# Kernel optimization log

Measured on AMD Instinct MI355X. Metric: run time of the kernel, lower is better.

## Reference

```python
import jax, jax.numpy as jnp
import numpy as np

EPS = 1e-5
K = 20


def _bn(x, gamma, beta):
    # BatchNorm in training mode: stats over all axes except last (channel)
    axes = tuple(range(x.ndim - 1))
    m = jnp.mean(x, axes, keepdims=True)
    v = jnp.var(x, axes, keepdims=True)
    return gamma * (x - m) * jax.lax.rsqrt(v + EPS) + beta


def _leaky(x):
    return jax.nn.leaky_relu(x, 0.2)


def _edge_conv(x, W, gamma, beta):
    # x: [B, N, C] channel-last. Faithful to source: topk on cdist with
    # torch default largest=True (k FARTHEST points). Squared distance
    # preserves the ordering of euclidean distance.
    sq = jnp.sum(x * x, axis=-1)                                    # [B,N]
    d2 = sq[:, :, None] + sq[:, None, :] - 2.0 * jnp.einsum('bnc,bmc->bnm', x, x)
    idx = jax.lax.top_k(d2, K)[1]                                   # [B,N,K]
    nbr = jax.vmap(lambda xi, ii: xi[ii])(x, idx)                   # [B,N,K,C]
    ctr = jnp.broadcast_to(x[:, :, None, :], nbr.shape)
    feat = jnp.concatenate([nbr - ctr, ctr], axis=-1)               # [B,N,K,2C]
    h = jnp.einsum('bnkc,oc->bnko', feat, W)                        # 1x1 conv
    return jnp.max(_leaky(_bn(h, gamma, beta)), axis=2)             # [B,N,O]


def _plane(x, w1, g1, b1, w2, g2, b2, w3, g3, b3, w4, g4, b4,
           w5, g5, b5, wl1, g6, b6, wl2, bl2, g7, b7):
    xt = jnp.transpose(x, (0, 2, 1))                                # [B,N,3]
    h1 = _edge_conv(xt, w1, g1, b1)                                 # [B,N,64]
    h2 = _edge_conv(h1, w2, g2, b2)                                 # [B,N,64]
    h3 = _edge_conv(h2, w3, g3, b3)                                 # [B,N,128]
    h4 = _edge_conv(h3, w4, g4, b4)                                 # [B,N,256]
    hc = jnp.concatenate([h1, h2, h3, h4], axis=-1)                 # [B,N,512]
    h = _leaky(_bn(jnp.einsum('bnc,oc->bno', hc, w5), g5, b5))      # [B,N,1024]
    pooled = jnp.concatenate([jnp.max(h, axis=1), jnp.mean(h, axis=1)], axis=-1)  # [B,2048]
    h = _leaky(_bn(pooled @ wl1.T, g6, b6))                         # [B,512]
    h = _leaky(_bn(h @ wl2.T + bl2, g7, b7))                        # [B,256]
    return h  # dropout p=0.0 -> identity


def setup_inputs() -> dict:
    key = jax.random.key(0)
    ks = jax.random.split(key, 16)
    B, N = 8, 2048
    f32 = jnp.float32
    d = {
        'x0': jax.random.normal(ks[0], (B, 3, N), f32),
        'x1': jax.random.normal(ks[1], (B, 3, N), f32),
        'x2': jax.random.normal(ks[2], (B, 3, N), f32),
        'w1': jax.random.normal(ks[3], (64, 6), f32) * 0.3,
        'w2': jax.random.normal(ks[4], (64, 128), f32) * 0.08,
        'w3': jax.random.normal(ks[5], (128, 128), f32) * 0.08,
        'w4': jax.random.normal(ks[6], (256, 256), f32) * 0.06,
        'w5': jax.random.normal(ks[7], (1024, 512), f32) * 0.04,
        'wl1': jax.random.normal(ks[8], (512, 2048), f32) * 0.02,
        'wl2': jax.random.normal(ks[9], (256, 512), f32) * 0.04,
        'bl2': jnp.zeros((256,), f32),
        'whead': jax.random.normal(ks[10], (7, 768), f32) * 0.03,
        'bhead': jnp.zeros((7,), f32),
    }
    for name, c in [('1', 64), ('2', 64), ('3', 128), ('4', 256), ('5', 1024),
                    ('6', 512), ('7', 256), ('8', 7)]:
        d['g' + name] = jnp.ones((c,), f32)
        d['b' + name] = jnp.zeros((c,), f32)
    return d


def reference(x0, x1, x2, w1, g1, b1, w2, g2, b2, w3, g3, b3, w4, g4, b4,
              w5, g5, b5, wl1, g6, b6, wl2, bl2, g7, b7, whead, bhead, g8, b8):
    feats = [
        _plane(x, w1, g1, b1, w2, g2, b2, w3, g3, b3, w4, g4, b4,
               w5, g5, b5, wl1, g6, b6, wl2, bl2, g7, b7)
        for x in (x0, x1, x2)
    ]
    h = jnp.concatenate(feats, axis=-1)                             # [B,768]
    # final MLP head: 1x1 conv on [B,768,1] + BN1d + ReLU + squeeze
    out = jnp.einsum('bc,oc->bo', h, whead) + bhead                 # [B,7]
    out = jax.nn.relu(_bn(out, g8, b8))
    return out
```

## Files before the change

kernel.cpp:

```cpp
#include <hip/hip_runtime.h>
#include <hip/hip_bf16.h>
#include <cstdint>
#include <cstddef>

constexpr int NB = 8;
constexpr int NP = 2048;
constexpr int BN = NB * NP;
constexpr int KK = 20;
constexpr float EPSBN = 1e-5f;
constexpr float NEG = -3.402823466e38f;
constexpr int SLOTS = 8;
constexpr int SLOTSM = 32;
constexpr int SLOTSW = 8;

typedef __attribute__((ext_vector_type(8))) short bf16x8;
typedef __attribute__((ext_vector_type(16))) float f32x16;

__device__ __forceinline__ float leaky(float x) { return x > 0.f ? x : 0.2f * x; }

__device__ __forceinline__ void split2(float x, unsigned short& h, unsigned short& l) {
    __hip_bfloat16 hh = __float2bfloat16(x);
    float hf = __bfloat162float(hh);
    __hip_bfloat16 ll = __float2bfloat16(x - hf);
    h = *reinterpret_cast<unsigned short*>(&hh);
    l = *reinterpret_cast<unsigned short*>(&ll);
}

__device__ __forceinline__ float b2f(unsigned short u) {
    __hip_bfloat16 h = *reinterpret_cast<__hip_bfloat16*>(&u);
    return __bfloat162float(h);
}

__device__ __forceinline__ unsigned int f2key(float f) {
    unsigned int u = __float_as_uint(f);
    return u ^ (unsigned int)(((int)u >> 31) | 0x80000000);
}

__global__ void k_transpose(const float* __restrict__ x, float* __restrict__ xt) {
    int i = blockIdx.x * 256 + threadIdx.x;
    if (i >= BN) return;
    int b = i >> 11, n = i & 2047;
    float4 v;
    v.x = x[(b * 3 + 0) * NP + n];
    v.y = x[(b * 3 + 1) * NP + n];
    v.z = x[(b * 3 + 2) * NP + n];
    v.w = 0.f;
    *(float4*)&xt[(size_t)i * 4] = v;
}

template <int CP4>
__global__ void k_sq4(const float4* __restrict__ FT4, float* __restrict__ sq) {
    int i = blockIdx.x * 256 + threadIdx.x;
    if (i >= BN) return;
    float s = 0.f;
#pragma unroll
    for (int cq = 0; cq < CP4; ++cq) {
        float4 f = FT4[(size_t)cq * BN + i];
        s += f.x * f.x + f.y * f.y + f.z * f.z + f.w * f.w;
    }
    sq[i] = s;
}

template <int CP>
__launch_bounds__(512, 4)
__global__ void k_knn2(const float4* __restrict__ FT4, const float* __restrict__ sq,
                       int* __restrict__ gidx) {
    constexpr int R = 8;
    constexpr int CP4 = CP / 4;
    __shared__ unsigned int ds[R][NP];
    int t = threadIdx.x;
    int b = blockIdx.x >> 8;
    int n0 = (blockIdx.x & 255) * R;
    const float4* FTb = FT4 + (size_t)b * NP;
    const float* sqb = sq + (size_t)b * NP;

    float acc[R][4];
#pragma unroll
    for (int r = 0; r < R; ++r)
#pragma unroll
        for (int mi = 0; mi < 4; ++mi) acc[r][mi] = 0.f;

    for (int cq = 0; cq < CP4; ++cq) {
        float4 f[4];
#pragma unroll
        for (int mi = 0; mi < 4; ++mi)
            f[mi] = FTb[(size_t)cq * BN + t + mi * 512];
#pragma unroll
        for (int r = 0; r < R; ++r) {
            float4 cv = FTb[(size_t)cq * BN + n0 + r];
#pragma unroll
            for (int mi = 0; mi < 4; ++mi)
                acc[r][mi] += f[mi].x * cv.x + f[mi].y * cv.y + f[mi].z * cv.z + f[mi].w * cv.w;
        }
    }
#pragma unroll
    for (int mi = 0; mi < 4; ++mi) {
        int m = t + mi * 512;
        float sm = sqb[m];
#pragma unroll
        for (int r = 0; r < R; ++r) ds[r][m] = f2key(sm - 2.f * acc[r][mi]);
    }
    __syncthreads();

    int wave = t >> 6, lane = t & 63;
    unsigned long long below = (1ull << lane) - 1ull;
    {
        int r = wave;
        unsigned int kv[32];
#pragma unroll
        for (int j = 0; j < 32; ++j) kv[j] = ds[r][lane + 64 * j];

        unsigned int T = 0;
        bool exact = false;
#pragma unroll 1
        for (int bit = 31; bit >= 0; --bit) {
            unsigned int tt = T | (1u << bit);
            int c = 0;
#pragma unroll
            for (int j = 0; j < 32; ++j)
                c += (int)__popcll(__ballot(kv[j] >= tt));
            if (c >= KK) {
                T = tt;
                if (c == KK) { exact = true; break; }
            }
        }

        int obase = (b * NP + n0 + r) * KK;
        if (exact) {
            int base = 0;
#pragma unroll 1
            for (int j = 0; j < 32; ++j) {
                bool pg = kv[j] >= T;
                unsigned long long mk = __ballot(pg);
                if (pg) gidx[obase + base + (int)__popcll(mk & below)] = lane + 64 * j;
                base += (int)__popcll(mk);
            }
        } else {
            int base = 0;
#pragma unroll 1
            for (int j = 0; j < 32; ++j) {
                bool pg = kv[j] > T;
                unsigned long long mk = __ballot(pg);
                if (pg) gidx[obase + base + (int)__popcll(mk & below)] = lane + 64 * j;
                base += (int)__popcll(mk);
            }
            int rem = KK - base;
#pragma unroll 1
            for (int j = 0; j < 32; ++j) {
                if (rem <= 0) break;
                bool pe = kv[j] == T;
                unsigned long long mk = __ballot(pe);
                int myp = (int)__popcll(mk & below);
                if (pe && myp < rem) gidx[obase + base + myp] = lane + 64 * j;
                int cnt = (int)__popcll(mk);
                int take = cnt < rem ? cnt : rem;
                base += take; rem -= take;
            }
        }
    }
}

__global__ void k_prepw(const float* __restrict__ W, int O, int Cact, int CP,
                        float* __restrict__ WaT, float* __restrict__ WdT) {
    int i = blockIdx.x * 256 + threadIdx.x;
    if (i >= CP * O) return;
    int c = i / O, o = i % O;
    float wa = (c < Cact) ? W[o * 2 * Cact + c] : 0.f;
    float wb = (c < Cact) ? W[o * 2 * Cact + Cact + c] : 0.f;
    WaT[i] = wa;
    WdT[i] = wb - wa;
}

__global__ void k_prepws2(const float* __restrict__ W, int O, int C,
                          unsigned short* __restrict__ WcH, unsigned short* __restrict__ WcL) {
    int i = blockIdx.x * 256 + threadIdx.x;
    if (i >= 2 * O * C) return;
    int r = i / C, k = i % C;
    float v;
    if (r < O) v = W[r * 2 * C + k];
    else {
        int o = r - O;
        v = W[o * 2 * C + C + k] - W[o * 2 * C + k];
    }
    split2(v, WcH[i], WcL[i]);
}

__global__ void k_splitw5(const float* __restrict__ w5, unsigned short* __restrict__ w5H,
                          unsigned short* __restrict__ w5L) {
    int i = blockIdx.x * 256 + threadIdx.x;
    if (i >= 1024 * 512) return;
    split2(w5[i], w5H[i], w5L[i]);
}

template <int O, int CP>
__launch_bounds__(O)
__global__ void k_conv(const float* __restrict__ F, int ld, const int* __restrict__ gidx,
                       const float* __restrict__ WaT, const float* __restrict__ WdT,
                       float* __restrict__ hmax, float* __restrict__ s1p,
                       float* __restrict__ s2p) {
    constexpr int CP4 = CP / 4;
    __shared__ float nbrT[2][CP][32];
    __shared__ float sctr[2][CP];
    __shared__ int sidx[2][KK];
    int t = threadIdx.x;
    int p0 = blockIdx.x * 2;
    int b = p0 >> 11;
    const float* Fb = F + (size_t)b * NP * ld;

    if (t < 2 * KK) {
        int pt = t / KK, k = t % KK;
        sidx[pt][k] = gidx[(size_t)(p0 + pt) * KK + k];
    }
    for (int e = t; e < 2 * CP; e += O) {
        int pt = e / CP, cc = e % CP;
        int n = (p0 + pt) & 2047;
        sctr[pt][cc] = Fb[(size_t)n * ld + cc];
    }
    __syncthreads();
    for (int e = t; e < 2 * KK * CP4; e += O) {
        int pt = e / (KK * CP4);
        int e2 = e % (KK * CP4);
        int k = e2 / CP4, cq = e2 % CP4;
        float4 f = *(const float4*)&Fb[(size_t)sidx[pt][k] * ld + cq * 4];
        int kp = (k + 4 * (cq & 7)) & 31;
        nbrT[pt][cq * 4 + 0][kp] = f.x;
        nbrT[pt][cq * 4 + 1][kp] = f.y;
        nbrT[pt][cq * 4 + 2][kp] = f.z;
        nbrT[pt][cq * 4 + 3][kp] = f.w;
    }
    __syncthreads();

    int o = t;
    float bacc0 = 0.f, bacc1 = 0.f;
#pragma unroll 4
    for (int c = 0; c < CP; ++c) {
        float w = WdT[c * O + o];
        bacc0 += sctr[0][c] * w;
        bacc1 += sctr[1][c] * w;
    }
    float a0[KK], a1[KK];
#pragma unroll
    for (int k = 0; k < KK; ++k) { a0[k] = 0.f; a1[k] = 0.f; }
#pragma unroll 2
    for (int c = 0; c < CP; ++c) {
        float w = WaT[c * O + o];
        int s = 4 * ((c >> 2) & 7);
#pragma unroll
        for (int kq = 0; kq < KK / 4; ++kq) {
            int kp = (4 * kq + s) & 31;
            float4 f0 = *(const float4*)&nbrT[0][c][kp];
            float4 f1 = *(const float4*)&nbrT[1][c][kp];
            a0[kq * 4 + 0] += w * f0.x; a1[kq * 4 + 0] += w * f1.x;
            a0[kq * 4 + 1] += w * f0.y; a1[kq * 4 + 1] += w * f1.y;
            a0[kq * 4 + 2] += w * f0.z; a1[kq * 4 + 2] += w * f1.z;
            a0[kq * 4 + 3] += w * f0.w; a1[kq * 4 + 3] += w * f1.w;
        }
    }
    float hm0 = NEG, hm1 = NEG, ts1 = 0.f, ts2 = 0.f;
#pragma unroll
    for (int k = 0; k < KK; ++k) {
        float h0 = a0[k] + bacc0;
        float h1 = a1[k] + bacc1;
        hm0 = fmaxf(hm0, h0); hm1 = fmaxf(hm1, h1);
        ts1 += h0 + h1; ts2 += h0 * h0 + h1 * h1;
    }
    hmax[(size_t)p0 * O + o] = hm0;
    hmax[(size_t)(p0 + 1) * O + o] = hm1;
    int slot = blockIdx.x & (SLOTS - 1);
    atomicAdd(&s1p[slot * O + o], ts1);
    atomicAdd(&s2p[slot * O + o], ts2);
}

template <int O, int C, int COFF>
__launch_bounds__(256, 4)
__global__ void k_gemms(const unsigned short* __restrict__ hcH,
                        const unsigned short* __restrict__ hcL,
                        const unsigned short* __restrict__ WdH,
                        const unsigned short* __restrict__ WdL,
                        float* __restrict__ bacc) {
    constexpr int KS = C / 16;
    int tid = threadIdx.x, wave = tid >> 6, lane = tid & 63;
    int row = lane & 31, half = lane >> 5;
    int p0 = blockIdx.x * 128 + wave * 32;
    int ob = blockIdx.y * 64;
    const unsigned short* aH = hcH + (size_t)(p0 + row) * 512 + COFF;
    const unsigned short* aL = hcL + (size_t)(p0 + row) * 512 + COFF;
    f32x16 acc[2];
#pragma unroll
    for (int nt = 0; nt < 2; ++nt)
#pragma unroll
        for (int r = 0; r < 16; ++r) acc[nt][r] = 0.f;

#pragma unroll 2
    for (int ks = 0; ks < KS; ++ks) {
        int k0 = ks * 16 + half * 8;
        bf16x8 avh = *(const bf16x8*)(aH + k0);
        bf16x8 avl = *(const bf16x8*)(aL + k0);
#pragma unroll
        for (int nt = 0; nt < 2; ++nt) {
            int j = ob + nt * 32 + row;
            bf16x8 bvh = *(const bf16x8*)(WdH + (size_t)j * C + k0);
            bf16x8 bvl = *(const bf16x8*)(WdL + (size_t)j * C + k0);
            acc[nt] = __builtin_amdgcn_mfma_f32_32x32x16_bf16(avh, bvh, acc[nt], 0, 0, 0);
            acc[nt] = __builtin_amdgcn_mfma_f32_32x32x16_bf16(avh, bvl, acc[nt], 0, 0, 0);
            acc[nt] = __builtin_amdgcn_mfma_f32_32x32x16_bf16(avl, bvh, acc[nt], 0, 0, 0);
        }
    }
#pragma unroll
    for (int nt = 0; nt < 2; ++nt)
#pragma unroll
        for (int r = 0; r < 16; ++r) {
            int i = (r & 3) + 8 * (r >> 2) + 4 * half;
            bacc[(size_t)(p0 + i) * O + ob + nt * 32 + row] = acc[nt][r];
        }
}

template <int O>
__launch_bounds__(256)
__global__ void k_gmax(const float* __restrict__ Gz, const int* __restrict__ gidx,
                       float* __restrict__ hmax, float* __restrict__ s1p,
                       float* __restrict__ s2p) {
    constexpr int PB = 256 / O;
    constexpr int O2 = 2 * O;
    __shared__ int sidx[PB][KK];
    int t = threadIdx.x;
    int pt = t / O, o = t % O;
    int p0 = blockIdx.x * PB;
    if (t < PB * KK) sidx[t / KK][t % KK] = gidx[(size_t)(p0 + t / KK) * KK + t % KK];
    __syncthreads();

    int p = p0 + pt;
    int b = p >> 11;
    const float* Gb = Gz + (size_t)b * 2048 * O2;
    float bacc = Gz[(size_t)p * O2 + O + o];
    float mx = NEG, ts1 = 0.f, ts2 = 0.f;
#pragma unroll 5
    for (int k = 0; k < KK; ++k) {
        float g = Gb[(size_t)sidx[pt][k] * O2 + o];
        float h = g + bacc;
        mx = fmaxf(mx, g);
        ts1 += h; ts2 += h * h;
    }
    hmax[(size_t)p * O + o] = mx + bacc;
    int slot = blockIdx.x & (SLOTSM - 1);
    atomicAdd(&s1p[slot * O + o], ts1);
    atomicAdd(&s2p[slot * O + o], ts2);
}

__global__ void k_redslots(const float* __restrict__ s1p, const float* __restrict__ s2p,
                           int O, int S, float* __restrict__ s1g, float* __restrict__ s2g) {
    int o = blockIdx.x * 256 + threadIdx.x;
    if (o >= O) return;
    float a = 0.f, c = 0.f;
    for (int s = 0; s < S; ++s) { a += s1p[s * O + o]; c += s2p[s * O + o]; }
    s1g[o] = a; s2g[o] = c;
}

__global__ void k_bnmax(const float* __restrict__ hmax, int O, const float* __restrict__ s1g,
                        const float* __restrict__ s2g, const float* __restrict__ gam,
                        const float* __restrict__ bet, unsigned short* __restrict__ outH,
                        unsigned short* __restrict__ outL, int ostride, int ooff,
                        float inv_cnt) {
    int i = blockIdx.x * 256 + threadIdx.x;
    if (i >= BN * O) return;
    int o = i % O, p = i / O;
    float m = s1g[o] * inv_cnt;
    float v = s2g[o] * inv_cnt - m * m;
    float rs = rsqrtf(v + EPSBN);
    float y = leaky(gam[o] * (hmax[i] - m) * rs + bet[o]);
    size_t oi = (size_t)p * ostride + ooff + o;
    split2(y, outH[oi], outL[oi]);
}

__global__ void k_pack4(const unsigned short* __restrict__ inH,
                        const unsigned short* __restrict__ inL, int coff,
                        float4* __restrict__ out) {
    __shared__ float tile[64][65];
    int tx = threadIdx.x & 63, ty = threadIdx.x >> 6;
    int p0 = blockIdx.x * 64, o0 = blockIdx.y * 64;
    for (int i = ty; i < 64; i += 4) {
        size_t idx = (size_t)(p0 + i) * 512 + coff + o0 + tx;
        tile[i][tx] = b2f(inH[idx]) + b2f(inL[idx]);
    }
    __syncthreads();
    for (int q = ty; q < 16; q += 4) {
        float4 v;
        v.x = tile[tx][4 * q + 0];
        v.y = tile[tx][4 * q + 1];
        v.z = tile[tx][4 * q + 2];
        v.w = tile[tx][4 * q + 3];
        out[(size_t)(o0 / 4 + q) * BN + p0 + tx] = v;
    }
}

__launch_bounds__(256, 2)
__global__ void k_w5ms(const unsigned short* __restrict__ hcH,
                       const unsigned short* __restrict__ hcL,
                       const unsigned short* __restrict__ w5H,
                       const unsigned short* __restrict__ w5L,
                       float* __restrict__ g5, float* __restrict__ s1p,
                       float* __restrict__ s2p) {
    int tid = threadIdx.x, wave = tid >> 6, lane = tid & 63;
    int row = lane & 31, half = lane >> 5;
    int p0 = blockIdx.x * 64;
    int ob = blockIdx.y * 512 + wave * 128;
    const unsigned short* aH0 = hcH + (size_t)(p0 + row) * 512;
    const unsigned short* aL0 = hcL + (size_t)(p0 + row) * 512;
    const unsigned short* aH1 = hcH + (size_t)(p0 + 32 + row) * 512;
    const unsigned short* aL1 = hcL + (size_t)(p0 + 32 + row) * 512;
    f32x16 acc0[4], acc1[4];
#pragma unroll
    for (int nt = 0; nt < 4; ++nt)
#pragma unroll
        for (int r = 0; r < 16; ++r) { acc0[nt][r] = 0.f; acc1[nt][r] = 0.f; }

#pragma unroll 2
    for (int ks = 0; ks < 32; ++ks) {
        int k0 = ks * 16 + half * 8;
        bf16x8 avh0 = *(const bf16x8*)(aH0 + k0);
        bf16x8 avl0 = *(const bf16x8*)(aL0 + k0);
        bf16x8 avh1 = *(const bf16x8*)(aH1 + k0);
        bf16x8 avl1 = *(const bf16x8*)(aL1 + k0);
#pragma unroll
        for (int nt = 0; nt < 4; ++nt) {
            int j = ob + nt * 32 + row;
            bf16x8 bvh = *(const bf16x8*)(w5H + (size_t)j * 512 + k0);
            bf16x8 bvl = *(const bf16x8*)(w5L + (size_t)j * 512 + k0);
            acc0[nt] = __builtin_amdgcn_mfma_f32_32x32x16_bf16(avh0, bvh, acc0[nt], 0, 0, 0);
            acc0[nt] = __builtin_amdgcn_mfma_f32_32x32x16_bf16(avh0, bvl, acc0[nt], 0, 0, 0);
            acc0[nt] = __builtin_amdgcn_mfma_f32_32x32x16_bf16(avl0, bvh, acc0[nt], 0, 0, 0);
            acc1[nt] = __builtin_amdgcn_mfma_f32_32x32x16_bf16(avh1, bvh, acc1[nt], 0, 0, 0);
            acc1[nt] = __builtin_amdgcn_mfma_f32_32x32x16_bf16(avh1, bvl, acc1[nt], 0, 0, 0);
            acc1[nt] = __builtin_amdgcn_mfma_f32_32x32x16_bf16(avl1, bvh, acc1[nt], 0, 0, 0);
        }
    }
    int slot = blockIdx.x & (SLOTSW - 1);
#pragma unroll
    for (int nt = 0; nt < 4; ++nt) {
        int j = ob + nt * 32 + row;
        float s10 = 0.f, s20 = 0.f, s11 = 0.f, s21 = 0.f;
#pragma unroll
        for (int r = 0; r < 16; ++r) {
            int i = (r & 3) + 8 * (r >> 2) + 4 * half;
            float v0 = acc0[nt][r];
            float v1 = acc1[nt][r];
            g5[(size_t)(p0 + i) * 1024 + j] = v0;
            g5[(size_t)(p0 + 32 + i) * 1024 + j] = v1;
            s10 += v0; s20 += v0 * v0;
            s11 += v1; s21 += v1 * v1;
        }
        s10 += __shfl_xor(s10, 32);
        s20 += __shfl_xor(s20, 32);
        s11 += __shfl_xor(s11, 32);
        s21 += __shfl_xor(s21, 32);
        if (half == 0) {
            atomicAdd(&s1p[slot * 1024 + j], s10 + s11);
            atomicAdd(&s2p[slot * 1024 + j], s20 + s21);
        }
    }
}

__global__ void k_pool(const float* __restrict__ gbuf, const float* __restrict__ s1g,
                       const float* __restrict__ s2g, const float* __restrict__ gam,
                       const float* __restrict__ bet, float* __restrict__ pmax,
                       float* __restrict__ psum) {
    int t = threadIdx.x;
    int blk = blockIdx.x;
    int nc = blk & 7, ot = (blk >> 3) & 3, b = blk >> 5;
    int o = ot * 256 + t;
    float m = s1g[o] * (1.f / 16384.f);
    float v = s2g[o] * (1.f / 16384.f) - m * m;
    float rs = rsqrtf(v + EPSBN);
    float ga = gam[o], be = bet[o];
    float vmax = NEG, vsum = 0.f;
    for (int j = 0; j < 256; ++j) {
        int n = nc * 256 + j;
        float x = gbuf[((size_t)b * NP + n) * 1024 + o];
        float y = leaky(ga * (x - m) * rs + be);
        vmax = fmaxf(vmax, y);
        vsum += y;
    }
    pmax[(b * 1024 + o) * 8 + nc] = vmax;
    psum[(b * 1024 + o) * 8 + nc] = vsum;
}

__global__ void k_poolfin(const float* __restrict__ pmax, const float* __restrict__ psum,
                          float* __restrict__ pooled) {
    int i = blockIdx.x * 256 + threadIdx.x;
    if (i >= 8192) return;
    float mx = NEG, sm = 0.f;
    for (int j = 0; j < 8; ++j) {
        mx = fmaxf(mx, pmax[i * 8 + j]);
        sm += psum[i * 8 + j];
    }
    int b = i >> 10, o = i & 1023;
    pooled[b * 2048 + o] = mx;
    pooled[b * 2048 + 1024 + o] = sm * (1.f / 2048.f);
}

template <int CIN>
__global__ void k_fc(const float* __restrict__ in, const float* __restrict__ W,
                     const float* __restrict__ bias, int O, float* __restrict__ z) {
    int i = blockIdx.x * 256 + threadIdx.x;
    if (i >= NB * O) return;
    int b = i / O, o = i % O;
    const float* wr = W + (size_t)o * CIN;
    const float* ir = in + (size_t)b * CIN;
    float acc = 0.f;
#pragma unroll 4
    for (int cq = 0; cq < CIN / 4; ++cq) {
        float4 wv = *(const float4*)&wr[cq * 4];
        float4 iv = *(const float4*)&ir[cq * 4];
        acc += wv.x * iv.x + wv.y * iv.y + wv.z * iv.z + wv.w * iv.w;
    }
    z[i] = acc + (bias ? bias[o] : 0.f);
}

__global__ void k_bnb(const float* __restrict__ z, int O, const float* __restrict__ gam,
                      const float* __restrict__ bet, float* __restrict__ out, int ostride,
                      int ooff) {
    int o = blockIdx.x * 256 + threadIdx.x;
    if (o >= O) return;
    float s1 = 0.f, s2 = 0.f;
#pragma unroll
    for (int b = 0; b < NB; ++b) {
        float x = z[b * O + o];
        s1 += x; s2 += x * x;
    }
    float m = s1 * 0.125f, v = s2 * 0.125f - m * m;
    float rs = rsqrtf(v + EPSBN);
    float ga = gam[o], be = bet[o];
    for (int b = 0; b < NB; ++b) {
        float y = ga * (z[b * O + o] - m) * rs + be;
        out[b * ostride + ooff + o] = leaky(y);
    }
}

__global__ void k_head(const float* __restrict__ hf, const float* __restrict__ wh,
                       const float* __restrict__ bh, const float* __restrict__ g8,
                       const float* __restrict__ b8, float* __restrict__ out) {
    __shared__ float zh[56];
    int t = threadIdx.x;
    if (t < 56) {
        int b = t / 7, o = t % 7;
        float acc = bh[o];
        for (int c = 0; c < 768; ++c) acc += hf[b * 768 + c] * wh[o * 768 + c];
        zh[t] = acc;
    }
    __syncthreads();
    if (t < 7) {
        float s1 = 0.f, s2 = 0.f;
        for (int b = 0; b < NB; ++b) {
            float x = zh[b * 7 + t];
            s1 += x; s2 += x * x;
        }
        float m = s1 * 0.125f, v = s2 * 0.125f - m * m;
        float rs = rsqrtf(v + EPSBN);
        for (int b = 0; b < NB; ++b) {
            float y = g8[t] * (zh[b * 7 + t] - m) * rs + b8[t];
            out[b * 7 + t] = fmaxf(y, 0.f);
        }
    }
}

extern "C" void kernel_launch(void* const* d_in, const int* in_sizes, int n_in, void* d_out,
                              int out_size, void* d_ws, size_t ws_size, hipStream_t stream) {
    const float* x[3] = {(const float*)d_in[0], (const float*)d_in[1], (const float*)d_in[2]};
    const float* w1 = (const float*)d_in[3];
    const float* w2 = (const float*)d_in[4];
    const float* w3 = (const float*)d_in[5];
    const float* w4 = (const float*)d_in[6];
    const float* w5 = (const float*)d_in[7];
    const float* wl1 = (const float*)d_in[8];
    const float* wl2 = (const float*)d_in[9];
    const float* bl2 = (const float*)d_in[10];
    const float* whead = (const float*)d_in[11];
    const float* bhead = (const float*)d_in[12];
    const float *g1 = (const float*)d_in[13], *b1 = (const float*)d_in[14];
    const float *g2 = (const float*)d_in[15], *b2 = (const float*)d_in[16];
    const float *g3 = (const float*)d_in[17], *b3 = (const float*)d_in[18];
    const float *g4 = (const float*)d_in[19], *b4 = (const float*)d_in[20];
    const float *g5 = (const float*)d_in[21], *b5 = (const float*)d_in[22];
    const float *g6 = (const float*)d_in[23], *b6 = (const float*)d_in[24];
    const float *g7 = (const float*)d_in[25], *b7 = (const float*)d_in[26];
    const float *g8 = (const float*)d_in[27], *b8 = (const float*)d_in[28];

    char* w = (char*)d_ws;
    auto alloc = [&](size_t bytes) {
        char* p = w;
        w += (bytes + 255) & ~(size_t)255;
        return p;
    };
    float* xt   = (float*)alloc((size_t)BN * 4 * 4);
    unsigned short* hcH = (unsigned short*)alloc((size_t)BN * 512 * 2);
    unsigned short* hcL = (unsigned short*)alloc((size_t)BN * 512 * 2);
    float4* ft4 = (float4*)alloc((size_t)32 * BN * 16);
    float* gbig = (float*)alloc((size_t)BN * 1024 * 4);
    int*   idx  = (int*)alloc((size_t)BN * KK * 4);
    float* sqv  = (float*)alloc((size_t)BN * 4);
    float* s1g  = (float*)alloc(1024 * 4);
    float* s2g  = (float*)alloc(1024 * 4);
    float* spart  = (float*)alloc(2 * SLOTS * 256 * 4);
    float* spartC = (float*)alloc(2 * SLOTSM * 256 * 4);
    float* spartW = (float*)alloc(2 * SLOTSW * 1024 * 4);
    float* pmax = (float*)alloc(8 * 1024 * 8 * 4);
    float* psum = (float*)alloc(8 * 1024 * 8 * 4);
    float* pooled = (float*)alloc(8 * 2048 * 4);
    float* z1 = (float*)alloc(8 * 512 * 4);
    float* a1 = (float*)alloc(8 * 512 * 4);
    float* z2 = (float*)alloc(8 * 256 * 4);
    float* hfeat = (float*)alloc(8 * 768 * 4);
    float* Wa1 = (float*)alloc(4 * 64 * 4);
    float* Wd1 = (float*)alloc(4 * 64 * 4);
    unsigned short* WcH2 = (unsigned short*)alloc(128 * 64 * 2);
    unsigned short* WcL2 = (unsigned short*)alloc(128 * 64 * 2);
    unsigned short* WcH3 = (unsigned short*)alloc(256 * 64 * 2);
    unsigned short* WcL3 = (unsigned short*)alloc(256 * 64 * 2);
    unsigned short* WcH4 = (unsigned short*)alloc(512 * 128 * 2);
    unsigned short* WcL4 = (unsigned short*)alloc(512 * 128 * 2);
    unsigned short* w5H  = (unsigned short*)alloc(1024 * 512 * 2);
    unsigned short* w5L  = (unsigned short*)alloc(1024 * 512 * 2);
    float* s1p = spart;
    float* s2p = spart + SLOTS * 256;
    float* s1pc = spartC;
    float* s2pc = spartC + SLOTSM * 256;
    float* s1pw = spartW;
    float* s2pw = spartW + SLOTSW * 1024;
    float* hmaxP = gbig + (size_t)BN * 512;

    k_prepw<<<(4 * 64 + 255) / 256, 256, 0, stream>>>(w1, 64, 3, 4, Wa1, Wd1);
    k_prepws2<<<(128 * 64 + 255) / 256, 256, 0, stream>>>(w2, 64, 64, WcH2, WcL2);
    k_prepws2<<<(256 * 64 + 255) / 256, 256, 0, stream>>>(w3, 128, 64, WcH3, WcL3);
    k_prepws2<<<(512 * 128 + 255) / 256, 256, 0, stream>>>(w4, 256, 128, WcH4, WcL4);
    k_splitw5<<<(1024 * 512) / 256, 256, 0, stream>>>(w5, w5H, w5L);

    const float inv_e = 1.f / (float)(BN * KK);
    for (int p = 0; p < 3; ++p) {
        k_transpose<<<BN / 256, 256, 0, stream>>>(x[p], xt);

        k_sq4<1><<<BN / 256, 256, 0, stream>>>((const float4*)xt, sqv);
        k_knn2<4><<<NB * (NP / 8), 512, 0, stream>>>((const float4*)xt, sqv, idx);
        hipMemsetAsync(spart, 0, 2 * SLOTS * 256 * 4, stream);
        k_conv<64, 4><<<BN / 2, 64, 0, stream>>>(xt, 4, idx, Wa1, Wd1, hmaxP, s1p, s2p);
        k_redslots<<<1, 256, 0, stream>>>(s1p, s2p, 64, SLOTS, s1g, s2g);
        k_bnmax<<<(BN * 64) / 256, 256, 0, stream>>>(hmaxP, 64, s1g, s2g, g1, b1, hcH, hcL, 512, 0, inv_e);
        k_pack4<<<dim3(BN / 64, 1), 256, 0, stream>>>(hcH, hcL, 0, ft4);

        k_sq4<16><<<BN / 256, 256, 0, stream>>>(ft4, sqv);
        k_knn2<64><<<NB * (NP / 8), 512, 0, stream>>>(ft4, sqv, idx);
        k_gemms<128, 64, 0><<<dim3(BN / 128, 2), 256, 0, stream>>>(hcH, hcL, WcH2, WcL2, gbig);
        hipMemsetAsync(spartC, 0, 2 * SLOTSM * 256 * 4, stream);
        k_gmax<64><<<BN / 4, 256, 0, stream>>>(gbig, idx, hmaxP, s1pc, s2pc);
        k_redslots<<<1, 256, 0, stream>>>(s1pc, s2pc, 64, SLOTSM, s1g, s2g);
        k_bnmax<<<(BN * 64) / 256, 256, 0, stream>>>(hmaxP, 64, s1g, s2g, g2, b2, hcH, hcL, 512, 64, inv_e);
        k_pack4<<<dim3(BN / 64, 1), 256, 0, stream>>>(hcH, hcL, 64, ft4);

        k_sq4<16><<<BN / 256, 256, 0, stream>>>(ft4, sqv);
        k_knn2<64><<<NB * (NP / 8), 512, 0, stream>>>(ft4, sqv, idx);
        k_gemms<256, 64, 64><<<dim3(BN / 128, 4), 256, 0, stream>>>(hcH, hcL, WcH3, WcL3, gbig);
        hipMemsetAsync(spartC, 0, 2 * SLOTSM * 256 * 4, stream);
        k_gmax<128><<<BN / 2, 256, 0, stream>>>(gbig, idx, hmaxP, s1pc, s2pc);
        k_redslots<<<1, 256, 0, stream>>>(s1pc, s2pc, 128, SLOTSM, s1g, s2g);
        k_bnmax<<<(BN * 128) / 256, 256, 0, stream>>>(hmaxP, 128, s1g, s2g, g3, b3, hcH, hcL, 512, 128, inv_e);
        k_pack4<<<dim3(BN / 64, 2), 256, 0, stream>>>(hcH, hcL, 128, ft4);

        k_sq4<32><<<BN / 256, 256, 0, stream>>>(ft4, sqv);
        k_knn2<128><<<NB * (NP / 8), 512, 0, stream>>>(ft4, sqv, idx);
        k_gemms<512, 128, 128><<<dim3(BN / 128, 8), 256, 0, stream>>>(hcH, hcL, WcH4, WcL4, gbig);
        hipMemsetAsync(spartC, 0, 2 * SLOTSM * 256 * 4, stream);
        k_gmax<256><<<BN, 256, 0, stream>>>(gbig, idx, hmaxP, s1pc, s2pc);
        k_redslots<<<1, 256, 0, stream>>>(s1pc, s2pc, 256, SLOTSM, s1g, s2g);
        k_bnmax<<<(BN * 256) / 256, 256, 0, stream>>>(hmaxP, 256, s1g, s2g, g4, b4, hcH, hcL, 512, 256, inv_e);

        hipMemsetAsync(spartW, 0, 2 * SLOTSW * 1024 * 4, stream);
        k_w5ms<<<dim3(BN / 64, 2), 256, 0, stream>>>(hcH, hcL, w5H, w5L, gbig, s1pw, s2pw);
        k_redslots<<<4, 256, 0, stream>>>(s1pw, s2pw, 1024, SLOTSW, s1g, s2g);
        k_pool<<<256, 256, 0, stream>>>(gbig, s1g, s2g, g5, b5, pmax, psum);
        k_poolfin<<<32, 256, 0, stream>>>(pmax, psum, pooled);

        k_fc<2048><<<(8 * 512 + 255) / 256, 256, 0, stream>>>(pooled, wl1, nullptr, 512, z1);
        k_bnb<<<2, 256, 0, stream>>>(z1, 512, g6, b6, a1, 512, 0);
        k_fc<512><<<(8 * 256 + 255) / 256, 256, 0, stream>>>(a1, wl2, bl2, 256, z2);
        k_bnb<<<1, 256, 0, stream>>>(z2, 256, g7, b7, hfeat, 768, p * 256);
    }
    k_head<<<1, 64, 0, stream>>>(hfeat, whead, bhead, g8, b8, (float*)d_out);
}
```

Before: 2.673 ms.

## Split fused KNN into separate gram-matrix and top-k selection kernels

The fused knn kernel for the 64- and 128-channel layers is replaced by two passes per half-batch. The first kernel computes distance keys and writes the full key matrix to a global scratch buffer instead of shared memory. The second kernel loads one row per wave and runs the radix top-20 selection with higher occupancy and no large shared-memory footprint. In exchange, a 4x2048x2048 key matrix is written to and read back from global memory, and there are extra kernel launches.

```diff
diff --git a/kernel.cpp b/kernel.cpp
--- a/kernel.cpp
+++ b/kernel.cpp
@@ -59,6 +59,56 @@
         s += f.x * f.x + f.y * f.y + f.z * f.z + f.w * f.w;
     }
     sq[i] = s;
+}
+
+__device__ __forceinline__ void select20(const unsigned int* kv, int lane,
+                                         unsigned long long below, int obase,
+                                         int* __restrict__ gidx) {
+    unsigned int T = 0;
+    bool exact = false;
+#pragma unroll 1
+    for (int bit = 31; bit >= 0; --bit) {
+        unsigned int tt = T | (1u << bit);
+        int c = 0;
+#pragma unroll
+        for (int j = 0; j < 32; ++j)
+            c += (int)__popcll(__ballot(kv[j] >= tt));
+        if (c >= KK) {
+            T = tt;
+            if (c == KK) { exact = true; break; }
+        }
+    }
+    if (exact) {
+        int base = 0;
+#pragma unroll 1
+        for (int j = 0; j < 32; ++j) {
+            bool pg = kv[j] >= T;
+            unsigned long long mk = __ballot(pg);
+            if (pg) gidx[obase + base + (int)__popcll(mk & below)] = lane + 64 * j;
+            base += (int)__popcll(mk);
+        }
+    } else {
+        int base = 0;
+#pragma unroll 1
+        for (int j = 0; j < 32; ++j) {
+            bool pg = kv[j] > T;
+            unsigned long long mk = __ballot(pg);
+            if (pg) gidx[obase + base + (int)__popcll(mk & below)] = lane + 64 * j;
+            base += (int)__popcll(mk);
+        }
+        int rem = KK - base;
+#pragma unroll 1
+        for (int j = 0; j < 32; ++j) {
+            if (rem <= 0) break;
+            bool pe = kv[j] == T;
+            unsigned long long mk = __ballot(pe);
+            int myp = (int)__popcll(mk & below);
+            if (pe && myp < rem) gidx[obase + base + myp] = lane + 64 * j;
+            int cnt = (int)__popcll(mk);
+            int take = cnt < rem ? cnt : rem;
+            base += take; rem -= take;
+        }
+    }
 }
 
 template <int CP>
@@ -109,55 +159,63 @@
         unsigned int kv[32];
 #pragma unroll
         for (int j = 0; j < 32; ++j) kv[j] = ds[r][lane + 64 * j];
-
-        unsigned int T = 0;
-        bool exact = false;
-#pragma unroll 1
-        for (int bit = 31; bit >= 0; --bit) {
-            unsigned int tt = T | (1u << bit);
-            int c = 0;
-#pragma unroll
-            for (int j = 0; j < 32; ++j)
-                c += (int)__popcll(__ballot(kv[j] >= tt));
-            if (c >= KK) {
-                T = tt;
-                if (c == KK) { exact = true; break; }
-            }
-        }
-
-        int obase = (b * NP + n0 + r) * KK;
-        if (exact) {
-            int base = 0;
-#pragma unroll 1
-            for (int j = 0; j < 32; ++j) {
-                bool pg = kv[j] >= T;
-                unsigned long long mk = __ballot(pg);
-                if (pg) gidx[obase + base + (int)__popcll(mk & below)] = lane + 64 * j;
-                base += (int)__popcll(mk);
-            }
-        } else {
-            int base = 0;
-#pragma unroll 1
-            for (int j = 0; j < 32; ++j) {
-                bool pg = kv[j] > T;
-                unsigned long long mk = __ballot(pg);
-                if (pg) gidx[obase + base + (int)__popcll(mk & below)] = lane + 64 * j;
-                base += (int)__popcll(mk);
-            }
-            int rem = KK - base;
-#pragma unroll 1
-            for (int j = 0; j < 32; ++j) {
-                if (rem <= 0) break;
-                bool pe = kv[j] == T;
-                unsigned long long mk = __ballot(pe);
-                int myp = (int)__popcll(mk & below);
-                if (pe && myp < rem) gidx[obase + base + myp] = lane + 64 * j;
-                int cnt = (int)__popcll(mk);
-                int take = cnt < rem ? cnt : rem;
-                base += take; rem -= take;
-            }
-        }
-    }
+        select20(kv, lane, below, (b * NP + n0 + r) * KK, gidx);
+    }
+}
+
+template <int CP>
+__launch_bounds__(512, 4)
+__global__ void k_gram(const float4* __restrict__ FT4, const float* __restrict__ sq,
+                       unsigned int* __restrict__ Gmat, int bbase) {
+    constexpr int R = 8;
+    constexpr int CP4 = CP / 4;
+    int t = threadIdx.x;
+    int bb = blockIdx.x >> 8;
+    int b = bbase + bb;
+    int n0 = (blockIdx.x & 255) * R;
+    const float4* FTb = FT4 + (size_t)b * NP;
+    const float* sqb = sq + (size_t)b * NP;
+
+    float acc[R][4];
+#pragma unroll
+    for (int r = 0; r < R; ++r)
+#pragma unroll
+        for (int mi = 0; mi < 4; ++mi) acc[r][mi] = 0.f;
+
+    for (int cq = 0; cq < CP4; ++cq) {
+        float4 f[4];
+#pragma unroll
+        for (int mi = 0; mi < 4; ++mi)
+            f[mi] = FTb[(size_t)cq * BN + t + mi * 512];
+#pragma unroll
+        for (int r = 0; r < R; ++r) {
+            float4 cv = FTb[(size_t)cq * BN + n0 + r];
+#pragma unroll
+            for (int mi = 0; mi < 4; ++mi)
+                acc[r][mi] += f[mi].x * cv.x + f[mi].y * cv.y + f[mi].z * cv.z + f[mi].w * cv.w;
+        }
+    }
+#pragma unroll
+    for (int mi = 0; mi < 4; ++mi) {
+        int m = t + mi * 512;
+        float sm = sqb[m];
+#pragma unroll
+        for (int r = 0; r < R; ++r)
+            Gmat[(size_t)(bb * NP + n0 + r) * NP + m] = f2key(sm - 2.f * acc[r][mi]);
+    }
+}
+
+__launch_bounds__(512, 8)
+__global__ void k_sel(const unsigned int* __restrict__ Gmat, int bbase,
+                      int* __restrict__ gidx) {
+    int t = threadIdx.x, wave = t >> 6, lane = t & 63;
+    int row = blockIdx.x * 8 + wave;
+    const unsigned int* Gr = Gmat + (size_t)row * NP;
+    unsigned int kv[32];
+#pragma unroll
+    for (int j = 0; j < 32; ++j) kv[j] = Gr[lane + 64 * j];
+    unsigned long long below = (1ull << lane) - 1ull;
+    select20(kv, lane, below, (bbase * NP + row) * KK, gidx);
 }
 
 __global__ void k_prepw(const float* __restrict__ W, int O, int Cact, int CP,
@@ -627,6 +685,7 @@
     float* s1pw = spartW;
     float* s2pw = spartW + SLOTSW * 1024;
     float* hmaxP = gbig + (size_t)BN * 512;
+    unsigned int* Gmat = (unsigned int*)gbig;
 
     k_prepw<<<(4 * 64 + 255) / 256, 256, 0, stream>>>(w1, 64, 3, 4, Wa1, Wd1);
     k_prepws2<<<(128 * 64 + 255) / 256, 256, 0, stream>>>(w2, 64, 64, WcH2, WcL2);
@@ -647,7 +706,10 @@
         k_pack4<<<dim3(BN / 64, 1), 256, 0, stream>>>(hcH, hcL, 0, ft4);
 
         k_sq4<16><<<BN / 256, 256, 0, stream>>>(ft4, sqv);
-        k_knn2<64><<<NB * (NP / 8), 512, 0, stream>>>(ft4, sqv, idx);
+        for (int hb = 0; hb < 2; ++hb) {
+            k_gram<64><<<1024, 512, 0, stream>>>(ft4, sqv, Gmat, hb * 4);
+            k_sel<<<1024, 512, 0, stream>>>(Gmat, hb * 4, idx);
+        }
         k_gemms<128, 64, 0><<<dim3(BN / 128, 2), 256, 0, stream>>>(hcH, hcL, WcH2, WcL2, gbig);
         hipMemsetAsync(spartC, 0, 2 * SLOTSM * 256 * 4, stream);
         k_gmax<64><<<BN / 4, 256, 0, stream>>>(gbig, idx, hmaxP, s1pc, s2pc);
@@ -656,7 +718,10 @@
         k_pack4<<<dim3(BN / 64, 1), 256, 0, stream>>>(hcH, hcL, 64, ft4);
 
         k_sq4<16><<<BN / 256, 256, 0, stream>>>(ft4, sqv);
-        k_knn2<64><<<NB * (NP / 8), 512, 0, stream>>>(ft4, sqv, idx);
+        for (int hb = 0; hb < 2; ++hb) {
+            k_gram<64><<<1024, 512, 0, stream>>>(ft4, sqv, Gmat, hb * 4);
+            k_sel<<<1024, 512, 0, stream>>>(Gmat, hb * 4, idx);
+        }
         k_gemms<256, 64, 64><<<dim3(BN / 128, 4), 256, 0, stream>>>(hcH, hcL, WcH3, WcL3, gbig);
         hipMemsetAsync(spartC, 0, 2 * SLOTSM * 256 * 4, stream);
         k_gmax<128><<<BN / 2, 256, 0, stream>>>(gbig, idx, hmaxP, s1pc, s2pc);
@@ -665,7 +730,10 @@
         k_pack4<<<dim3(BN / 64, 2), 256, 0, stream>>>(hcH, hcL, 128, ft4);
 
         k_sq4<32><<<BN / 256, 256, 0, stream>>>(ft4, sqv);
-        k_knn2<128><<<NB * (NP / 8), 512, 0, stream>>>(ft4, sqv, idx);
+        for (int hb = 0; hb < 2; ++hb) {
+            k_gram<128><<<1024, 512, 0, stream>>>(ft4, sqv, Gmat, hb * 4);
+            k_sel<<<1024, 512, 0, stream>>>(Gmat, hb * 4, idx);
+        }
         k_gemms<512, 128, 128><<<dim3(BN / 128, 8), 256, 0, stream>>>(hcH, hcL, WcH4, WcL4, gbig);
         hipMemsetAsync(spartC, 0, 2 * SLOTSM * 256 * 4, stream);
         k_gmax<256><<<BN, 256, 0, stream>>>(gbig, idx, hmaxP, s1pc, s2pc);
```

New measurement: 3.185 ms. +19.1%, slower.
